# Performance work log

Hardware: AMD Instinct MI355X
Metric: run time of the kernel (lower is better)

Reference implementation:

```python
import jax, jax.numpy as jnp
import numpy as np

B, T, C = 2, 2048, 1024
N_HEAD = 16
HEAD_DIM = C // N_HEAD


def setup_inputs() -> dict:
    key = jax.random.key(0)
    k1, k2, k3 = jax.random.split(key, 3)
    x = jax.random.normal(k1, (B, T, C), dtype=jnp.float32)
    w_attn = jax.random.normal(k2, (C, 3 * C), dtype=jnp.float32) * 0.02
    b_attn = jnp.zeros((3 * C,), dtype=jnp.float32)
    w_proj = jax.random.normal(k3, (C, C), dtype=jnp.float32) * 0.02
    b_proj = jnp.zeros((C,), dtype=jnp.float32)
    return {"x": x, "w_attn": w_attn, "b_attn": b_attn, "w_proj": w_proj, "b_proj": b_proj}


def reference(x, w_attn, b_attn, w_proj, b_proj):
    Bz, Tz, Cz = x.shape
    qkv = x @ w_attn + b_attn                       # [B, T, 3C]
    q, k, v = jnp.split(qkv, 3, axis=-1)
    # [B, H, T, D]
    q = q.reshape(Bz, Tz, N_HEAD, HEAD_DIM).transpose(0, 2, 1, 3)
    k = k.reshape(Bz, Tz, N_HEAD, HEAD_DIM).transpose(0, 2, 1, 3)
    v = v.reshape(Bz, Tz, N_HEAD, HEAD_DIM).transpose(0, 2, 1, 3)
    scale = 1.0 / np.sqrt(HEAD_DIM).astype(np.float32)
    att = jnp.einsum('bhqd,bhkd->bhqk', q, k) * scale  # [B, H, T, T]
    causal = jnp.tril(jnp.ones((Tz, Tz), dtype=bool))
    att = jnp.where(causal[None, None], att, -jnp.inf)
    att = jax.nn.softmax(att, axis=-1)
    y = jnp.einsum('bhqk,bhkd->bhqd', att, v)          # [B, H, T, D]
    y = y.transpose(0, 2, 1, 3).reshape(Bz, Tz, Cz)
    return y @ w_proj + b_proj
```

## Files before the change

### kernel.cpp

```cpp
#include <hip/hip_runtime.h>
#include <stdint.h>

#define T_SEQ 2048
#define NH 16
#define HD 64
#define M_DIM 4096
#define K_DIM 1024

typedef __attribute__((ext_vector_type(8))) short bf16x8;
typedef __attribute__((ext_vector_type(4))) float f32x4;
typedef __attribute__((ext_vector_type(4))) unsigned short u16x4;

__device__ __forceinline__ unsigned short f2bf(float f) {
  union { float f; uint32_t u; } x; x.f = f;
  uint32_t u = x.u;
  return (unsigned short)((u + 0x7fffu + ((u >> 16) & 1u)) >> 16);
}

__device__ __forceinline__ uint32_t cvtpk_bf16(float a, float b) {
  uint32_t r;
  asm("v_cvt_pk_bf16_f32 %0, %1, %2" : "=v"(r) : "v"(a), "v"(b));
  return r;
}

#define GLOAD16(g, l) __builtin_amdgcn_global_load_lds( \
    (const __attribute__((address_space(1))) unsigned int*)(g), \
    (__attribute__((address_space(3))) unsigned int*)(l), 16, 0, 0)

__device__ __forceinline__ void do_convert(const float* __restrict__ src,
                                           unsigned short* __restrict__ dst, int bid) {
  int idx = (bid * 256 + threadIdx.x) * 4;
  f32x4 v = *(const f32x4*)(src + idx);
  u16x4 o;
  #pragma unroll
  for (int i = 0; i < 4; ++i) o[i] = f2bf(v[i]);
  *(u16x4*)(dst + idx) = o;
}

__device__ __forceinline__ void do_transpose(const float* __restrict__ src,
                                             unsigned short* __restrict__ dst,
                                             int R, int Cn, int bx, int by,
                                             float (*tile)[65]) {
  const int r0 = by * 64, c0 = bx * 64;
  const int t = threadIdx.x;
  const int rr = t >> 4;
  const int c4 = (t & 15) * 4;
  #pragma unroll
  for (int p = 0; p < 4; ++p) {
    f32x4 v = *(const f32x4*)(src + (size_t)(r0 + p * 16 + rr) * Cn + c0 + c4);
    #pragma unroll
    for (int i = 0; i < 4; ++i) tile[p * 16 + rr][c4 + i] = v[i];
  }
  __syncthreads();
  #pragma unroll
  for (int p = 0; p < 4; ++p) {
    const int cl = p * 16 + rr;
    u16x4 o;
    #pragma unroll
    for (int i = 0; i < 4; ++i) o[i] = f2bf(tile[c4 + i][cl]);
    *(u16x4*)(dst + (size_t)(c0 + cl) * R + r0 + c4) = o;
  }
}

__global__ __launch_bounds__(256) void prep_kernel(
    const float* __restrict__ x, unsigned short* __restrict__ xb,
    const float* __restrict__ w_attn, unsigned short* __restrict__ wqkvT,
    const float* __restrict__ w_proj, unsigned short* __restrict__ wprojT) {
  __shared__ float tile[64][65];
  const int b = blockIdx.x;
  if (b < 4096) {
    do_convert(x, xb, b);
  } else if (b < 4096 + 768) {
    const int bid = b - 4096;
    do_transpose(w_attn, wqkvT, 1024, 3072, bid % 48, bid / 48, tile);
  } else {
    const int bid = b - 4864;
    do_transpose(w_proj, wprojT, 1024, 1024, bid % 16, bid / 16, tile);
  }
}

template <int MODE, int WM>
__global__ __launch_bounds__(WM * 128) void gemm2_kernel(
    const unsigned short* __restrict__ A,
    const unsigned short* __restrict__ Bt,
    const float* __restrict__ bias,
    unsigned short* __restrict__ qout,
    unsigned short* __restrict__ kout,
    unsigned short* __restrict__ vTout,
    float* __restrict__ fout) {
  constexpr int BM = WM * 64;
  constexpr int NT = WM * 128;
  constexpr int U_A = BM * 4;
  constexpr int NU = (U_A + 512) / NT;
  __shared__ __align__(16) unsigned short As[2][BM * 32];
  __shared__ __align__(16) unsigned short Bs[2][128 * 32];
  const int t = threadIdx.x;
  const int w = t >> 6, l = t & 63;
  const int wr = w >> 1, wc = w & 1;
  const int lr = l & 15, lg = l >> 4;
  const int br = blockIdx.y, bc = blockIdx.x;

  f32x4 acc[4][4];
  const f32x4 zf = {0.f, 0.f, 0.f, 0.f};
  #pragma unroll
  for (int i = 0; i < 4; ++i)
    #pragma unroll
    for (int j = 0; j < 4; ++j) acc[i][j] = zf;

  const unsigned short* Abase = A + (size_t)(br * BM) * K_DIM;
  const unsigned short* Bbase = Bt + (size_t)(bc * 128) * K_DIM;

  #define STAGE(k0, buf) do {                                                    \
    _Pragma("unroll")                                                            \
    for (int i = 0; i < NU; ++i) {                                               \
      const int u = i * NT + t;                                                  \
      if (u < U_A) {                                                             \
        GLOAD16(Abase + (size_t)(u >> 2) * K_DIM + (k0) + (u & 3) * 8,           \
                &As[buf][u * 8]);                                                \
      } else {                                                                   \
        const int v = u - U_A;                                                   \
        GLOAD16(Bbase + (size_t)(v >> 2) * K_DIM + (k0) + (v & 3) * 8,           \
                &Bs[buf][v * 8]);                                                \
      }                                                                          \
    }                                                                            \
  } while (0)

  #define COMPUTE(buf) do {                                                      \
    bf16x8 af[4], bfv[4];                                                        \
    _Pragma("unroll")                                                            \
    for (int f = 0; f < 4; ++f) {                                                \
      af[f]  = *(const bf16x8*)(&As[buf][(wr * 64 + f * 16 + lr) * 32 + lg * 8]);\
      bfv[f] = *(const bf16x8*)(&Bs[buf][(wc * 64 + f * 16 + lr) * 32 + lg * 8]);\
    }                                                                            \
    _Pragma("unroll")                                                            \
    for (int fr = 0; fr < 4; ++fr)                                               \
      _Pragma("unroll")                                                          \
      for (int fc = 0; fc < 4; ++fc)                                             \
        acc[fr][fc] = __builtin_amdgcn_mfma_f32_16x16x32_bf16(af[fr], bfv[fc],   \
                                                              acc[fr][fc], 0, 0, 0); \
  } while (0)

  STAGE(0, 0);
  __syncthreads();
  #pragma unroll 1
  for (int k0 = 0; k0 < K_DIM; k0 += 64) {
    if (k0 + 32 < K_DIM) STAGE(k0 + 32, 1);
    COMPUTE(0);
    __syncthreads();
    if (k0 + 64 < K_DIM) STAGE(k0 + 64, 0);
    COMPUTE(1);
    __syncthreads();
  }
  #undef STAGE
  #undef COMPUTE

  #pragma unroll
  for (int fr = 0; fr < 4; ++fr) {
    #pragma unroll
    for (int fc = 0; fc < 4; ++fc) {
      const int m0 = br * BM + wr * 64 + fr * 16 + lg * 4;
      const int n  = bc * 128 + wc * 64 + fc * 16 + lr;
      if (MODE == 0) {
        const int which = n >> 10, rem = n & 1023;
        const int h = rem >> 6, d = rem & 63;
        const int b = m0 >> 11, tt0 = m0 & 2047;
        const int bh = b * NH + h;
        if (which == 2) {
          u16x4 pack;
          #pragma unroll
          for (int r = 0; r < 4; ++r) pack[r] = f2bf(acc[fr][fc][r] + bias[n]);
          *(u16x4*)(vTout + ((size_t)bh * HD + d) * T_SEQ + tt0) = pack;
        } else {
          unsigned short* o = (which == 0) ? qout : kout;
          const float sc = (which == 0) ? 0.18033688011112042f : 1.0f;
          #pragma unroll
          for (int r = 0; r < 4; ++r)
            o[((size_t)bh * T_SEQ + tt0 + r) * HD + d] = f2bf((acc[fr][fc][r] + bias[n]) * sc);
        }
      } else {
        #pragma unroll
        for (int r = 0; r < 4; ++r)
          fout[(size_t)(m0 + r) * 1024 + n] = acc[fr][fc][r] + bias[n];
      }
    }
  }
}

__global__ __launch_bounds__(256) void flash_attn_kernel(
    const unsigned short* __restrict__ qg,
    const unsigned short* __restrict__ kg,
    const unsigned short* __restrict__ vTg,
    unsigned short* __restrict__ yg) {
  __shared__ __align__(16) unsigned short Ks[2][64 * 64];
  __shared__ __align__(16) unsigned short Vs[2][64 * 64];
  __shared__ __align__(16) unsigned short P[4][16][64];

  const int t = threadIdx.x;
  const int w = t >> 6, l = t & 63;
  const int lr = l & 15, lg = l >> 4;
  const int lb = (blockIdx.x & 7) * 64 + (blockIdx.x >> 3);
  const int pid = lb & 15;
  const int bh = lb >> 4;
  const int swz = lr & 7;

  const int srow0 = t >> 3;
  const int sch = t & 7;

  const size_t kgb = (size_t)bh * T_SEQ * HD;
  const size_t vgb = (size_t)bh * HD * T_SEQ;
  const f32x4 zf = {0.f, 0.f, 0.f, 0.f};

  #pragma unroll 1
  for (int ph = 0; ph < 2; ++ph) {
    const int qt = ph ? (31 - pid) : pid;
    const int nt = qt + 1;
    const int qw = qt * 64 + w * 16;
    const int qrow = qw + lr;

    const size_t qoff = ((size_t)bh * T_SEQ + qw + lr) * HD + lg * 8;
    const bf16x8 qf0 = *(const bf16x8*)(qg + qoff);
    const bf16x8 qf1 = *(const bf16x8*)(qg + qoff + 32);

    f32x4 acc[4];
    #pragma unroll
    for (int i = 0; i < 4; ++i) acc[i] = zf;
    float m_run = 0.f;
    float l_part = 0.f;

    #pragma unroll
    for (int sh = 0; sh < 2; ++sh) {
      const int row = sh * 32 + srow0;
      const int sc = (sch ^ (row & 7)) * 8;
      GLOAD16(kg + kgb + (size_t)row * HD + sc, Ks[0] + row * 64 + sch * 8);
      GLOAD16(vTg + vgb + (size_t)row * T_SEQ + sc, Vs[0] + row * 64 + sch * 8);
    }
    __syncthreads();

    int cur = 0;
    #pragma unroll 1
    for (int it = 0; it < nt; ++it) {
      const int kv0 = it * 64;
      if (it + 1 < nt) {
        const int kvn = kv0 + 64;
        #pragma unroll
        for (int sh = 0; sh < 2; ++sh) {
          const int row = sh * 32 + srow0;
          const int sc = (sch ^ (row & 7)) * 8;
          GLOAD16(kg + kgb + (size_t)(kvn + row) * HD + sc, Ks[cur ^ 1] + row * 64 + sch * 8);
          GLOAD16(vTg + vgb + (size_t)row * T_SEQ + kvn + sc, Vs[cur ^ 1] + row * 64 + sch * 8);
        }
      }

      f32x4 s[4];
      __builtin_amdgcn_s_setprio(1);
      #pragma unroll
      for (int fc = 0; fc < 4; ++fc) {
        const unsigned short* kr = Ks[cur] + (fc * 16 + lr) * 64;
        const bf16x8 k0v = *(const bf16x8*)(kr + ((lg ^ swz) * 8));
        const bf16x8 k1v = *(const bf16x8*)(kr + (((lg + 4) ^ swz) * 8));
        f32x4 sv = zf;
        sv = __builtin_amdgcn_mfma_f32_16x16x32_bf16(k0v, qf0, sv, 0, 0, 0);
        sv = __builtin_amdgcn_mfma_f32_16x16x32_bf16(k1v, qf1, sv, 0, 0, 0);
        s[fc] = sv;
      }
      __builtin_amdgcn_s_setprio(0);

      if (it == nt - 1) {
        #pragma unroll
        for (int fc = 0; fc < 4; ++fc)
          #pragma unroll
          for (int r = 0; r < 4; ++r) {
            const int tkv = kv0 + fc * 16 + lg * 4 + r;
            if (tkv > qrow) s[fc][r] = -1e30f;
          }
      }

      float mt = s[0][0];
      #pragma unroll
      for (int fc = 0; fc < 4; ++fc)
        #pragma unroll
        for (int r = 0; r < 4; ++r) mt = fmaxf(mt, s[fc][r]);
      if (__any(mt > m_run + 8.f)) {
        float mrow = fmaxf(mt, __shfl_xor(mt, 16));
        mrow = fmaxf(mrow, __shfl_xor(mrow, 32));
        const float m_new = fmaxf(m_run, mrow);
        const float fac = __builtin_amdgcn_exp2f(m_run - m_new);
        l_part *= fac;
        float frs[4];
        #pragma unroll
        for (int r = 0; r < 4; ++r) frs[r] = __shfl(fac, lg * 4 + r);
        #pragma unroll
        for (int fd = 0; fd < 4; ++fd)
          #pragma unroll
          for (int r = 0; r < 4; ++r) acc[fd][r] *= frs[r];
        m_run = m_new;
      }

      #pragma unroll
      for (int fc = 0; fc < 4; ++fc) {
        float e0 = __builtin_amdgcn_exp2f(s[fc][0] - m_run);
        float e1 = __builtin_amdgcn_exp2f(s[fc][1] - m_run);
        float e2 = __builtin_amdgcn_exp2f(s[fc][2] - m_run);
        float e3 = __builtin_amdgcn_exp2f(s[fc][3] - m_run);
        l_part += (e0 + e1) + (e2 + e3);
        uint2 pk;
        pk.x = cvtpk_bf16(e0, e1);
        pk.y = cvtpk_bf16(e2, e3);
        *(uint2*)&P[w][lr][(fc * 16 + lg * 4) ^ ((lr & 3) << 4)] = pk;
      }

      const bf16x8 pa0 = *(const bf16x8*)&P[w][lr][(lg * 8) ^ ((lr & 3) << 4)];
      const bf16x8 pa1 = *(const bf16x8*)&P[w][lr][(32 + lg * 8) ^ ((lr & 3) << 4)];
      __builtin_amdgcn_s_setprio(1);
      #pragma unroll
      for (int fd = 0; fd < 4; ++fd) {
        const unsigned short* vr = Vs[cur] + (fd * 16 + lr) * 64;
        const bf16x8 v0 = *(const bf16x8*)(vr + ((lg ^ swz) * 8));
        const bf16x8 v1 = *(const bf16x8*)(vr + (((lg + 4) ^ swz) * 8));
        acc[fd] = __builtin_amdgcn_mfma_f32_16x16x32_bf16(pa0, v0, acc[fd], 0, 0, 0);
        acc[fd] = __builtin_amdgcn_mfma_f32_16x16x32_bf16(pa1, v1, acc[fd], 0, 0, 0);
      }
      __builtin_amdgcn_s_setprio(0);
      __syncthreads();
      cur ^= 1;
    }

    float lsum = l_part;
    lsum += __shfl_xor(lsum, 16);
    lsum += __shfl_xor(lsum, 32);

    const int b = bh >> 4, h = bh & 15;
    #pragma unroll
    for (int r = 0; r < 4; ++r) {
      const float lv = __shfl(lsum, lg * 4 + r);
      const float linv = 1.f / lv;
      const int tt = qw + lg * 4 + r;
      #pragma unroll
      for (int fd = 0; fd < 4; ++fd) {
        const int d = fd * 16 + lr;
        yg[(((size_t)b * T_SEQ + tt) * NH + h) * HD + d] = f2bf(acc[fd][r] * linv);
      }
    }
    __syncthreads();
  }
}

extern "C" void kernel_launch(void* const* d_in, const int* in_sizes, int n_in,
                              void* d_out, int out_size, void* d_ws, size_t ws_size,
                              hipStream_t stream) {
  (void)in_sizes; (void)n_in; (void)out_size; (void)ws_size;
  const float* x      = (const float*)d_in[0];
  const float* w_attn = (const float*)d_in[1];
  const float* b_attn = (const float*)d_in[2];
  const float* w_proj = (const float*)d_in[3];
  const float* b_proj = (const float*)d_in[4];
  float* out = (float*)d_out;

  char* ws = (char*)d_ws;
  unsigned short* xb     = (unsigned short*)(ws);
  unsigned short* wqkvT  = (unsigned short*)(ws + (8ull  << 20));
  unsigned short* wprojT = (unsigned short*)(ws + (14ull << 20));
  unsigned short* qb     = (unsigned short*)(ws + (16ull << 20));
  unsigned short* kb     = (unsigned short*)(ws + (24ull << 20));
  unsigned short* vT     = (unsigned short*)(ws + (32ull << 20));
  unsigned short* yb     = (unsigned short*)(ws + (40ull << 20));

  prep_kernel<<<5120, 256, 0, stream>>>(x, xb, w_attn, wqkvT, w_proj, wprojT);
  gemm2_kernel<0, 4><<<dim3(24, 16), 512, 0, stream>>>(xb, wqkvT, b_attn, qb, kb, vT, nullptr);
  flash_attn_kernel<<<512, 256, 0, stream>>>(qb, kb, vT, yb);
  gemm2_kernel<1, 2><<<dim3(8, 32), 256, 0, stream>>>(yb, wprojT, b_proj, nullptr, nullptr, nullptr, out);
}
```

Measured before the change: 189.9 us.

## Keep P in registers via 16x16x16 MFMA and launch one q-tile per block

The attention kernel no longer stages the softmax probabilities P through shared memory. The exp results are packed into bf16x4 registers and fed straight into v_mfma_f32_16x16x16_bf16, with V fragments read at 4-element granularity to match that layout. The paired-tile loop (pid and 31-pid in one block) is replaced by one query tile per block over 1024 blocks ordered heaviest-first, and launch_bounds now requests 4 blocks per SIMD. The QKV GEMM also switches to a smaller 256-thread configuration with twice as many blocks. The trade-offs are half-width MFMAs, more LDS reads for V, and possible load imbalance from dropping the causal pairing.

```diff
diff --git a/kernel.cpp b/kernel.cpp
--- a/kernel.cpp
+++ b/kernel.cpp
@@ -8,6 +8,7 @@
 #define K_DIM 1024
 
 typedef __attribute__((ext_vector_type(8))) short bf16x8;
+typedef __attribute__((ext_vector_type(4))) short bf16x4;
 typedef __attribute__((ext_vector_type(4))) float f32x4;
 typedef __attribute__((ext_vector_type(4))) unsigned short u16x4;
 
@@ -21,6 +22,11 @@
   uint32_t r;
   asm("v_cvt_pk_bf16_f32 %0, %1, %2" : "=v"(r) : "v"(a), "v"(b));
   return r;
+}
+
+__device__ __forceinline__ f32x4 mfma16(bf16x4 a, bf16x4 b, f32x4 c) {
+  asm("v_mfma_f32_16x16x16_bf16 %0, %1, %2, %0" : "+v"(c) : "v"(a), "v"(b));
+  return c;
 }
 
 #define GLOAD16(g, l) __builtin_amdgcn_global_load_lds( \
@@ -186,21 +192,23 @@
   }
 }
 
-__global__ __launch_bounds__(256) void flash_attn_kernel(
+__global__ __launch_bounds__(256, 4) void flash_attn_kernel(
     const unsigned short* __restrict__ qg,
     const unsigned short* __restrict__ kg,
     const unsigned short* __restrict__ vTg,
     unsigned short* __restrict__ yg) {
   __shared__ __align__(16) unsigned short Ks[2][64 * 64];
   __shared__ __align__(16) unsigned short Vs[2][64 * 64];
-  __shared__ __align__(16) unsigned short P[4][16][64];
 
   const int t = threadIdx.x;
   const int w = t >> 6, l = t & 63;
   const int lr = l & 15, lg = l >> 4;
-  const int lb = (blockIdx.x & 7) * 64 + (blockIdx.x >> 3);
-  const int pid = lb & 15;
-  const int bh = lb >> 4;
+  const int i = blockIdx.x;
+  const int bh = (i & 7) * 4 + ((i >> 3) & 3);
+  const int qt = 31 - (i >> 5);
+  const int nt = qt + 1;
+  const int qw = qt * 64 + w * 16;
+  const int qrow = qw + lr;
   const int swz = lr & 7;
 
   const int srow0 = t >> 3;
@@ -210,138 +218,132 @@
   const size_t vgb = (size_t)bh * HD * T_SEQ;
   const f32x4 zf = {0.f, 0.f, 0.f, 0.f};
 
+  const size_t qoff = ((size_t)bh * T_SEQ + qw + lr) * HD + lg * 8;
+  const bf16x8 qf0 = *(const bf16x8*)(qg + qoff);
+  const bf16x8 qf1 = *(const bf16x8*)(qg + qoff + 32);
+
+  f32x4 acc[4];
+  #pragma unroll
+  for (int k = 0; k < 4; ++k) acc[k] = zf;
+  float m_run = 0.f;
+  float l_part = 0.f;
+
+  #pragma unroll
+  for (int sh = 0; sh < 2; ++sh) {
+    const int row = sh * 32 + srow0;
+    const int sc = (sch ^ (row & 7)) * 8;
+    GLOAD16(kg + kgb + (size_t)row * HD + sc, Ks[0] + row * 64 + sch * 8);
+    GLOAD16(vTg + vgb + (size_t)row * T_SEQ + sc, Vs[0] + row * 64 + sch * 8);
+  }
+  __syncthreads();
+
+  int cur = 0;
   #pragma unroll 1
-  for (int ph = 0; ph < 2; ++ph) {
-    const int qt = ph ? (31 - pid) : pid;
-    const int nt = qt + 1;
-    const int qw = qt * 64 + w * 16;
-    const int qrow = qw + lr;
-
-    const size_t qoff = ((size_t)bh * T_SEQ + qw + lr) * HD + lg * 8;
-    const bf16x8 qf0 = *(const bf16x8*)(qg + qoff);
-    const bf16x8 qf1 = *(const bf16x8*)(qg + qoff + 32);
-
-    f32x4 acc[4];
-    #pragma unroll
-    for (int i = 0; i < 4; ++i) acc[i] = zf;
-    float m_run = 0.f;
-    float l_part = 0.f;
-
-    #pragma unroll
-    for (int sh = 0; sh < 2; ++sh) {
-      const int row = sh * 32 + srow0;
-      const int sc = (sch ^ (row & 7)) * 8;
-      GLOAD16(kg + kgb + (size_t)row * HD + sc, Ks[0] + row * 64 + sch * 8);
-      GLOAD16(vTg + vgb + (size_t)row * T_SEQ + sc, Vs[0] + row * 64 + sch * 8);
-    }
-    __syncthreads();
-
-    int cur = 0;
-    #pragma unroll 1
-    for (int it = 0; it < nt; ++it) {
-      const int kv0 = it * 64;
-      if (it + 1 < nt) {
-        const int kvn = kv0 + 64;
-        #pragma unroll
-        for (int sh = 0; sh < 2; ++sh) {
-          const int row = sh * 32 + srow0;
-          const int sc = (sch ^ (row & 7)) * 8;
-          GLOAD16(kg + kgb + (size_t)(kvn + row) * HD + sc, Ks[cur ^ 1] + row * 64 + sch * 8);
-          GLOAD16(vTg + vgb + (size_t)row * T_SEQ + kvn + sc, Vs[cur ^ 1] + row * 64 + sch * 8);
-        }
+  for (int it = 0; it < nt; ++it) {
+    const int kv0 = it * 64;
+    if (it + 1 < nt) {
+      const int kvn = kv0 + 64;
+      #pragma unroll
+      for (int sh = 0; sh < 2; ++sh) {
+        const int row = sh * 32 + srow0;
+        const int sc = (sch ^ (row & 7)) * 8;
+        GLOAD16(kg + kgb + (size_t)(kvn + row) * HD + sc, Ks[cur ^ 1] + row * 64 + sch * 8);
+        GLOAD16(vTg + vgb + (size_t)row * T_SEQ + kvn + sc, Vs[cur ^ 1] + row * 64 + sch * 8);
       }
-
-      f32x4 s[4];
-      __builtin_amdgcn_s_setprio(1);
-      #pragma unroll
-      for (int fc = 0; fc < 4; ++fc) {
-        const unsigned short* kr = Ks[cur] + (fc * 16 + lr) * 64;
-        const bf16x8 k0v = *(const bf16x8*)(kr + ((lg ^ swz) * 8));
-        const bf16x8 k1v = *(const bf16x8*)(kr + (((lg + 4) ^ swz) * 8));
-        f32x4 sv = zf;
-        sv = __builtin_amdgcn_mfma_f32_16x16x32_bf16(k0v, qf0, sv, 0, 0, 0);
-        sv = __builtin_amdgcn_mfma_f32_16x16x32_bf16(k1v, qf1, sv, 0, 0, 0);
-        s[fc] = sv;
-      }
-      __builtin_amdgcn_s_setprio(0);
-
-      if (it == nt - 1) {
-        #pragma unroll
-        for (int fc = 0; fc < 4; ++fc)
-          #pragma unroll
-          for (int r = 0; r < 4; ++r) {
-            const int tkv = kv0 + fc * 16 + lg * 4 + r;
-            if (tkv > qrow) s[fc][r] = -1e30f;
-          }
-      }
-
-      float mt = s[0][0];
+    }
+
+    f32x4 s[4];
+    __builtin_amdgcn_s_setprio(1);
+    #pragma unroll
+    for (int fc = 0; fc < 4; ++fc) {
+      const unsigned short* kr = Ks[cur] + (fc * 16 + lr) * 64;
+      const bf16x8 k0v = *(const bf16x8*)(kr + ((lg ^ swz) * 8));
+      const bf16x8 k1v = *(const bf16x8*)(kr + (((lg + 4) ^ swz) * 8));
+      f32x4 sv = zf;
+      sv = __builtin_amdgcn_mfma_f32_16x16x32_bf16(k0v, qf0, sv, 0, 0, 0);
+      sv = __builtin_amdgcn_mfma_f32_16x16x32_bf16(k1v, qf1, sv, 0, 0, 0);
+      s[fc] = sv;
+    }
+    __builtin_amdgcn_s_setprio(0);
+
+    if (it == nt - 1) {
       #pragma unroll
       for (int fc = 0; fc < 4; ++fc)
         #pragma unroll
-        for (int r = 0; r < 4; ++r) mt = fmaxf(mt, s[fc][r]);
-      if (__any(mt > m_run + 8.f)) {
-        float mrow = fmaxf(mt, __shfl_xor(mt, 16));
-        mrow = fmaxf(mrow, __shfl_xor(mrow, 32));
-        const float m_new = fmaxf(m_run, mrow);
-        const float fac = __builtin_amdgcn_exp2f(m_run - m_new);
-        l_part *= fac;
-        float frs[4];
+        for (int r = 0; r < 4; ++r) {
+          const int tkv = kv0 + fc * 16 + lg * 4 + r;
+          if (tkv > qrow) s[fc][r] = -1e30f;
+        }
+    }
+
+    float mt = s[0][0];
+    #pragma unroll
+    for (int fc = 0; fc < 4; ++fc)
+      #pragma unroll
+      for (int r = 0; r < 4; ++r) mt = fmaxf(mt, s[fc][r]);
+    if (__any(mt > m_run + 8.f)) {
+      float mrow = fmaxf(mt, __shfl_xor(mt, 16));
+      mrow = fmaxf(mrow, __shfl_xor(mrow, 32));
+      const float m_new = fmaxf(m_run, mrow);
+      const float fac = __builtin_amdgcn_exp2f(m_run - m_new);
+      l_part *= fac;
+      float frs[4];
+      #pragma unroll
+      for (int r = 0; r < 4; ++r) frs[r] = __shfl(fac, lg * 4 + r);
+      #pragma unroll
+      for (int fd = 0; fd < 4; ++fd)
         #pragma unroll
-        for (int r = 0; r < 4; ++r) frs[r] = __shfl(fac, lg * 4 + r);
-        #pragma unroll
-        for (int fd = 0; fd < 4; ++fd)
-          #pragma unroll
-          for (int r = 0; r < 4; ++r) acc[fd][r] *= frs[r];
-        m_run = m_new;
+        for (int r = 0; r < 4; ++r) acc[fd][r] *= frs[r];
+      m_run = m_new;
+    }
+
+    union { uint32_t d[2]; bf16x4 v; } pkd[4];
+    #pragma unroll
+    for (int fc = 0; fc < 4; ++fc) {
+      float e0 = __builtin_amdgcn_exp2f(s[fc][0] - m_run);
+      float e1 = __builtin_amdgcn_exp2f(s[fc][1] - m_run);
+      float e2 = __builtin_amdgcn_exp2f(s[fc][2] - m_run);
+      float e3 = __builtin_amdgcn_exp2f(s[fc][3] - m_run);
+      l_part += (e0 + e1) + (e2 + e3);
+      pkd[fc].d[0] = cvtpk_bf16(e0, e1);
+      pkd[fc].d[1] = cvtpk_bf16(e2, e3);
+    }
+
+    __builtin_amdgcn_s_setprio(1);
+    #pragma unroll
+    for (int fd = 0; fd < 4; ++fd) {
+      const unsigned short* vr = Vs[cur] + (fd * 16 + lr) * 64;
+      bf16x4 vf[4];
+      #pragma unroll
+      for (int fc = 0; fc < 4; ++fc) {
+        const int ch = (fc * 2 + (lg >> 1)) ^ swz;
+        vf[fc] = *(const bf16x4*)(vr + ch * 8 + (lg & 1) * 4);
       }
-
-      #pragma unroll
-      for (int fc = 0; fc < 4; ++fc) {
-        float e0 = __builtin_amdgcn_exp2f(s[fc][0] - m_run);
-        float e1 = __builtin_amdgcn_exp2f(s[fc][1] - m_run);
-        float e2 = __builtin_amdgcn_exp2f(s[fc][2] - m_run);
-        float e3 = __builtin_amdgcn_exp2f(s[fc][3] - m_run);
-        l_part += (e0 + e1) + (e2 + e3);
-        uint2 pk;
-        pk.x = cvtpk_bf16(e0, e1);
-        pk.y = cvtpk_bf16(e2, e3);
-        *(uint2*)&P[w][lr][(fc * 16 + lg * 4) ^ ((lr & 3) << 4)] = pk;
-      }
-
-      const bf16x8 pa0 = *(const bf16x8*)&P[w][lr][(lg * 8) ^ ((lr & 3) << 4)];
-      const bf16x8 pa1 = *(const bf16x8*)&P[w][lr][(32 + lg * 8) ^ ((lr & 3) << 4)];
-      __builtin_amdgcn_s_setprio(1);
-      #pragma unroll
-      for (int fd = 0; fd < 4; ++fd) {
-        const unsigned short* vr = Vs[cur] + (fd * 16 + lr) * 64;
-        const bf16x8 v0 = *(const bf16x8*)(vr + ((lg ^ swz) * 8));
-        const bf16x8 v1 = *(const bf16x8*)(vr + (((lg + 4) ^ swz) * 8));
-        acc[fd] = __builtin_amdgcn_mfma_f32_16x16x32_bf16(pa0, v0, acc[fd], 0, 0, 0);
-        acc[fd] = __builtin_amdgcn_mfma_f32_16x16x32_bf16(pa1, v1, acc[fd], 0, 0, 0);
-      }
-      __builtin_amdgcn_s_setprio(0);
-      __syncthreads();
-      cur ^= 1;
-    }
-
-    float lsum = l_part;
-    lsum += __shfl_xor(lsum, 16);
-    lsum += __shfl_xor(lsum, 32);
-
-    const int b = bh >> 4, h = bh & 15;
-    #pragma unroll
-    for (int r = 0; r < 4; ++r) {
-      const float lv = __shfl(lsum, lg * 4 + r);
-      const float linv = 1.f / lv;
-      const int tt = qw + lg * 4 + r;
-      #pragma unroll
-      for (int fd = 0; fd < 4; ++fd) {
-        const int d = fd * 16 + lr;
-        yg[(((size_t)b * T_SEQ + tt) * NH + h) * HD + d] = f2bf(acc[fd][r] * linv);
-      }
-    }
+      f32x4 a = acc[fd];
+      #pragma unroll
+      for (int fc = 0; fc < 4; ++fc) a = mfma16(pkd[fc].v, vf[fc], a);
+      acc[fd] = a;
+    }
+    __builtin_amdgcn_s_setprio(0);
     __syncthreads();
+    cur ^= 1;
+  }
+
+  float lsum = l_part;
+  lsum += __shfl_xor(lsum, 16);
+  lsum += __shfl_xor(lsum, 32);
+
+  const int b = bh >> 4, h = bh & 15;
+  #pragma unroll
+  for (int r = 0; r < 4; ++r) {
+    const float lv = __shfl(lsum, lg * 4 + r);
+    const float linv = 1.f / lv;
+    const int tt = qw + lg * 4 + r;
+    #pragma unroll
+    for (int fd = 0; fd < 4; ++fd) {
+      const int d = fd * 16 + lr;
+      yg[(((size_t)b * T_SEQ + tt) * NH + h) * HD + d] = f2bf(acc[fd][r] * linv);
+    }
   }
 }
 
@@ -366,7 +368,7 @@
   unsigned short* yb     = (unsigned short*)(ws + (40ull << 20));
 
   prep_kernel<<<5120, 256, 0, stream>>>(x, xb, w_attn, wqkvT, w_proj, wprojT);
-  gemm2_kernel<0, 4><<<dim3(24, 16), 512, 0, stream>>>(xb, wqkvT, b_attn, qb, kb, vT, nullptr);
-  flash_attn_kernel<<<512, 256, 0, stream>>>(qb, kb, vT, yb);
+  gemm2_kernel<0, 2><<<dim3(24, 32), 256, 0, stream>>>(xb, wqkvT, b_attn, qb, kb, vT, nullptr);
+  flash_attn_kernel<<<1024, 256, 0, stream>>>(qb, kb, vT, yb);
   gemm2_kernel<1, 2><<<dim3(8, 32), 256, 0, stream>>>(yb, wprojT, b_proj, nullptr, nullptr, nullptr, out);
 }
```

Measured after the change: 193.7 us. 2.0% more time.
